# Performance work log

Hardware: AMD Instinct MI355X
Metric: run time of the kernel (lower is better)

The kernel has to match this reference:

```python
import jax, jax.numpy as jnp
import numpy as np
import math

B, T = 32, 64
VOCAB = 50005
EMB = 512
HID = 1024
SES = 1024
KNOW = 8785
NEG = math.exp(-100)

def _glorot(key, shape):
    fan_in, fan_out = shape[1], shape[0]
    lim = (6.0 / (fan_in + fan_out)) ** 0.5
    return jax.random.uniform(key, shape, jnp.float32, -lim, lim)

def setup_inputs() -> dict:
    key = jax.random.key(0)
    ks = jax.random.split(key, 16)
    inp = {}
    inp['ses_encoding'] = jax.random.normal(ks[0], (B, 1, SES), jnp.float32)
    inp['know_encoding'] = jax.random.normal(ks[1], (B, 1, SES), jnp.float32)
    inp['target'] = jax.random.randint(ks[2], (B, T), 0, 50000)
    inp['embed_w'] = jax.random.normal(ks[3], (VOCAB, EMB), jnp.float32) * 0.02
    # GRU params (PyTorch layout: W_ih [3H, E], W_hh [3H, H], gate order r,z,n)
    s = 1.0 / (HID ** 0.5)
    inp['W_ih'] = jax.random.uniform(ks[4], (3 * HID, EMB), jnp.float32, -s, s)
    inp['W_hh'] = jax.random.uniform(ks[5], (3 * HID, HID), jnp.float32, -s, s)
    inp['b_ih'] = jax.random.uniform(ks[6], (3 * HID,), jnp.float32, -s, s)
    inp['b_hh'] = jax.random.uniform(ks[7], (3 * HID,), jnp.float32, -s, s)
    inp['ses_to_dec_w'] = _glorot(ks[8], (HID, SES))
    inp['ses_to_dec_b'] = jnp.zeros((HID,), jnp.float32)
    inp['dec_inf_w'] = _glorot(ks[9], (2 * EMB, HID))
    inp['ses_inf_w'] = _glorot(ks[10], (2 * EMB, SES))
    inp['emb_inf_w'] = _glorot(ks[11], (2 * EMB, EMB))
    inp['emb_inf_b'] = jnp.zeros((2 * EMB,), jnp.float32)
    inp['W1'] = jax.random.normal(ks[12], (VOCAB, SES), jnp.float32) * 0.02
    inp['W2'] = jax.random.normal(ks[13], (VOCAB, SES), jnp.float32) * 0.02
    inp['W3'] = jax.random.normal(ks[14], (VOCAB, 2 * EMB), jnp.float32) * 0.02
    inp['W4'] = jax.random.normal(ks[15], (VOCAB, EMB), jnp.float32) * 0.02
    inp['know_vote_w'] = _glorot(jax.random.fold_in(key, 99), (KNOW, SES))
    return inp

def _gru_step(x, h, W_ih, W_hh, b_ih, b_hh):
    # x: [B,E], h: [B,H]
    gi = x @ W_ih.T + b_ih
    gh = h @ W_hh.T + b_hh
    ir, iz, inn = jnp.split(gi, 3, axis=-1)
    hr, hz, hn = jnp.split(gh, 3, axis=-1)
    r = jax.nn.sigmoid(ir + hr)
    z = jax.nn.sigmoid(iz + hz)
    n = jnp.tanh(inn + r * hn)
    return (1.0 - z) * h + z * n  # torch: h' = (1-z)*n + z*h with torch z; note torch formula

def _gru_step_torch(x, h, W_ih, W_hh, b_ih, b_hh):
    gi = x @ W_ih.T + b_ih
    gh = h @ W_hh.T + b_hh
    ir, iz, inn = jnp.split(gi, 3, axis=-1)
    hr, hz, hn = jnp.split(gh, 3, axis=-1)
    r = jax.nn.sigmoid(ir + hr)
    z = jax.nn.sigmoid(iz + hz)
    n = jnp.tanh(inn + r * hn)
    return (1.0 - z) * n + z * h

def reference(ses_encoding, know_encoding, target, embed_w, W_ih, W_hh, b_ih, b_hh,
              ses_to_dec_w, ses_to_dec_b, dec_inf_w, ses_inf_w, emb_inf_w, emb_inf_b,
              W1, W2, W3, W4, know_vote_w):
    ses = ses_encoding[:, 0, :]    # [B, SES]
    know = know_encoding[:, 0, :]  # [B, SES]
    target_emb = embed_w[target]   # [B, T, E]

    h0 = jnp.tanh(ses @ ses_to_dec_w.T + ses_to_dec_b)  # [B, H]

    # time-invariant pieces
    ses_inf_vec = ses @ ses_inf_w.T                      # [B, 2E]
    l1 = ses @ W1.T                                      # [B, V]
    l2 = know @ W2.T                                     # [B, V]
    # knowledge mixture log-probs (constant over time)
    ks = know @ know_vote_w.T                            # [B, KNOW]
    ks = ks[:, :-1]                                      # drop last -> [B, KNOW-1]
    pad_l = jnp.full((ks.shape[0], 10), NEG, ks.dtype)
    pad_r = jnp.full((ks.shape[0], VOCAB - 10 - (KNOW - 1)), NEG, ks.dtype)
    know_scores = jnp.concatenate([pad_l, ks, pad_r], axis=1)  # [B, V]
    know_probs = jax.nn.log_softmax(know_scores, axis=-1)      # [B, V]
    gate_const = l1 + l2                                 # [B, V]

    def step(h, emb_t):
        # emb_t: [B, E]
        h_new = _gru_step_torch(emb_t, h, W_ih, W_hh, b_ih, b_hh)  # [B, H]
        dec_hid_vec = h_new @ dec_inf_w.T                          # [B, 2E]
        target_inf = emb_t @ emb_inf_w.T + emb_inf_b               # [B, 2E]
        total = dec_hid_vec + ses_inf_vec + target_inf             # [B, 2E]
        mx = jnp.max(total.reshape(total.shape[0], EMB, 2), axis=-1)  # maxout -> [B, E]
        logits = mx @ embed_w.T                                    # shared embedding -> [B, V]
        hid_probs = jax.nn.log_softmax(logits, axis=-1)
        l3 = h_new @ W3.T                                          # note: W3 applied to hid_o [B,H]... but W3 is [V,2E]
        l4 = emb_t @ W4.T                                          # [B, V]
        gate = jax.nn.sigmoid(gate_const + l3 + l4)                # [B, V]
        final = gate * hid_probs + (1.0 - gate) * know_probs       # [B, V]
        return h_new, final

    # target_emb time-major for scan
    _, outs = jax.lax.scan(step, h0, jnp.swapaxes(target_emb, 0, 1))
    final_scores_all = jnp.swapaxes(outs, 0, 1)  # [B, T, V]
    return final_scores_all
```

## Files before the change

### kernel.cpp

```cpp
#include <hip/hip_runtime.h>

constexpr int VOC  = 50005;
constexpr int VOCP = 50048;
constexpr int VOCP2= 50176;
constexpr int NTM  = 391;
constexpr int NTMP = 400;
constexpr int KSN  = 8784;
constexpr float NPAD = 41221.0f;

typedef unsigned short u16;
typedef __attribute__((ext_vector_type(4))) float f32x4;
typedef __attribute__((ext_vector_type(8))) short bf16x8;

__device__ __forceinline__ float dot4(float4 a, float4 b) {
    return a.x*b.x + a.y*b.y + a.z*b.z + a.w*b.w;
}
__device__ __forceinline__ float sigmoidf_(float x) { return 1.0f / (1.0f + expf(-x)); }
__device__ __forceinline__ u16 f2bf(float f) {
    unsigned x = __float_as_uint(f);
    return (u16)((x + 0x7FFFu + ((x >> 16) & 1u)) >> 16);
}
__device__ __forceinline__ float bf2f(u16 u) { return __uint_as_float(((unsigned)u) << 16); }
__device__ __forceinline__ bf16x8 pack8(float4 lo, float4 hi) {
    union { bf16x8 v; unsigned u[4]; } r;
    r.u[0] = f2bf(lo.x) | ((unsigned)f2bf(lo.y) << 16);
    r.u[1] = f2bf(lo.z) | ((unsigned)f2bf(lo.w) << 16);
    r.u[2] = f2bf(hi.x) | ((unsigned)f2bf(hi.y) << 16);
    r.u[3] = f2bf(hi.z) | ((unsigned)f2bf(hi.w) << 16);
    return r.v;
}
template<int AUX>
__device__ __forceinline__ void gload_lds16x(const void* g, void* l) {
    __builtin_amdgcn_global_load_lds((const __attribute__((address_space(1))) unsigned int*)g,
                                     (__attribute__((address_space(3))) unsigned int*)l, 16, 0, AUX);
}
__device__ __forceinline__ void gload_lds16(const void* g, void* l) { gload_lds16x<0>(g, l); }
__device__ __forceinline__ void store_u16_sc(u16* p, u16 v) {
    asm volatile("global_store_short %0, %1, off sc0 sc1" :: "v"(p), "v"((unsigned)v) : "memory");
}
__device__ __forceinline__ void cvt4(const float* src, u16* dst) {
    float4 v = *(const float4*)src;
    unsigned lo = f2bf(v.x) | ((unsigned)f2bf(v.y) << 16);
    unsigned hi = f2bf(v.z) | ((unsigned)f2bf(v.w) << 16);
    *(uint2*)dst = make_uint2(lo, hi);
}

__global__ __launch_bounds__(256) void k_cvt(const float* __restrict__ src, u16* __restrict__ dst,
                                             int ncols, int sld, int dld) {
    int row = blockIdx.x;
    int c = (blockIdx.y * 256 + threadIdx.x) * 4;
    if (c >= ncols) return;
    cvt4(src + (size_t)row * sld + c, dst + (size_t)row * dld + c);
}

__global__ __launch_bounds__(256) void k_bsk(const float* __restrict__ ses,
                                             const float* __restrict__ know,
                                             u16* __restrict__ Bsk) {
    int row = blockIdx.x;
    for (int c0 = threadIdx.x * 4; c0 < 2048; c0 += 1024) {
        uint2 val = make_uint2(0, 0);
        if (row < 32) {
            const float* srcp = (c0 < 1024) ? ses + (size_t)row * 1024 + c0
                                            : know + (size_t)row * 1024 + (c0 - 1024);
            float4 v = *(const float4*)srcp;
            val = make_uint2(f2bf(v.x) | ((unsigned)f2bf(v.y) << 16),
                             f2bf(v.z) | ((unsigned)f2bf(v.w) << 16));
        }
        *(uint2*)(Bsk + (size_t)row * 2048 + c0) = val;
    }
}

__global__ __launch_bounds__(128) void k_gather(const float* __restrict__ embed,
                                                const int* __restrict__ target,
                                                u16* __restrict__ BG) {
    int n = blockIdx.x;
    int row = target[n];
    int c = threadIdx.x * 4;
    cvt4(embed + (size_t)row * 512 + c, BG + (size_t)n * 1536 + 1024 + c);
}

__global__ __launch_bounds__(256) void k_h0_sesinf(const float* __restrict__ ses,
                                                   const float* __restrict__ sdw,
                                                   const float* __restrict__ sdb,
                                                   const float* __restrict__ siw,
                                                   float* __restrict__ h0,
                                                   float* __restrict__ sesinf) {
    int g = blockIdx.x * 256 + threadIdx.x;
    int b = g & 31;
    int jg = g >> 5;
    int j0 = jg * 4;
    const float4* s4 = (const float4*)(ses + (size_t)b * 1024);
    const float4* wa[4];
    const float4* wc[4];
#pragma unroll
    for (int r = 0; r < 4; ++r) {
        wa[r] = (const float4*)(sdw + (size_t)(j0 + r) * 1024);
        wc[r] = (const float4*)(siw + (size_t)(j0 + r) * 1024);
    }
    float a[4] = {0, 0, 0, 0}, c[4] = {0, 0, 0, 0};
    for (int kq = 0; kq < 256; ++kq) {
        float4 sv = s4[kq];
#pragma unroll
        for (int r = 0; r < 4; ++r) { a[r] += dot4(sv, wa[r][kq]); c[r] += dot4(sv, wc[r][kq]); }
    }
#pragma unroll
    for (int r = 0; r < 4; ++r) {
        h0[b * 1024 + j0 + r] = tanhf(a[r] + sdb[j0 + r]);
        sesinf[b * 1024 + j0 + r] = c[r];
    }
}

__global__ __launch_bounds__(256) void k_lseknow(const float* __restrict__ ks,
                                                 float* __restrict__ lsek) {
    int b = blockIdx.x;
    int t = threadIdx.x;
    __shared__ float sm[256];
    float m = -1e30f;
    for (int j = t; j < KSN; j += 256) m = fmaxf(m, ks[(size_t)b * KSN + j]);
    sm[t] = m;
    __syncthreads();
    for (int s = 128; s > 0; s >>= 1) { if (t < s) sm[t] = fmaxf(sm[t], sm[t + s]); __syncthreads(); }
    m = fmaxf(sm[0], 0.0f);
    __syncthreads();
    float s = 0.0f;
    for (int j = t; j < KSN; j += 256) s += expf(ks[(size_t)b * KSN + j] - m);
    sm[t] = s;
    __syncthreads();
    for (int r = 128; r > 0; r >>= 1) { if (t < r) sm[t] += sm[t + r]; __syncthreads(); }
    if (t == 0) lsek[b] = m + logf(sm[0] + NPAD * expf(0.0f - m));
}

template<int MODE>
__global__ __launch_bounds__(128) void k_sk32(const float* __restrict__ A1,
                                              const float* __restrict__ A2,
                                              const u16* __restrict__ Bsk,
                                              float* __restrict__ outp) {
    const int lane = threadIdx.x & 63;
    const int w = threadIdx.x >> 6;
    const int lrow = lane & 15;
    const int kg = lane >> 4;
    constexpr int K = (MODE == 0) ? 2048 : 1024;
    constexpr int bc0 = (MODE == 0) ? 0 : 1024;
    const int rowmax = (MODE == 0) ? (VOC - 1) : (KSN - 1);
    const int vb = blockIdx.x * 64 + w * 32;
    const int r0 = min(vb + lrow, rowmax);
    const int r1 = min(vb + 16 + lrow, rowmax);
    f32x4 acc[2][2] = {{{0.f,0.f,0.f,0.f},{0.f,0.f,0.f,0.f}},
                       {{0.f,0.f,0.f,0.f},{0.f,0.f,0.f,0.f}}};
    for (int k0 = 0; k0 < K; k0 += 32) {
        int kc = k0 + kg * 8;
        const float* s0;
        const float* s1;
        if (MODE == 0 && k0 >= 1024) {
            s0 = A2 + (size_t)r0 * 1024 + (kc - 1024);
            s1 = A2 + (size_t)r1 * 1024 + (kc - 1024);
        } else {
            s0 = A1 + (size_t)r0 * 1024 + kc;
            s1 = A1 + (size_t)r1 * 1024 + kc;
        }
        bf16x8 af0 = pack8(*(const float4*)s0, *(const float4*)(s0 + 4));
        bf16x8 af1 = pack8(*(const float4*)s1, *(const float4*)(s1 + 4));
        bf16x8 b0 = *(const bf16x8*)(Bsk + (size_t)lrow * 2048 + bc0 + kc);
        bf16x8 b1 = *(const bf16x8*)(Bsk + (size_t)(16 + lrow) * 2048 + bc0 + kc);
        acc[0][0] = __builtin_amdgcn_mfma_f32_16x16x32_bf16(af0, b0, acc[0][0], 0, 0, 0);
        acc[0][1] = __builtin_amdgcn_mfma_f32_16x16x32_bf16(af0, b1, acc[0][1], 0, 0, 0);
        acc[1][0] = __builtin_amdgcn_mfma_f32_16x16x32_bf16(af1, b0, acc[1][0], 0, 0, 0);
        acc[1][1] = __builtin_amdgcn_mfma_f32_16x16x32_bf16(af1, b1, acc[1][1], 0, 0, 0);
    }
    const int rg = kg * 4;
#pragma unroll
    for (int mi = 0; mi < 2; ++mi)
#pragma unroll
        for (int ni = 0; ni < 2; ++ni)
#pragma unroll
            for (int r = 0; r < 4; ++r) {
                int v = vb + mi * 16 + rg + r;
                int b = ni * 16 + lrow;
                if (MODE == 0) outp[(size_t)b * VOCP2 + v] = acc[mi][ni][r];
                else if (v < KSN) outp[(size_t)b * KSN + v] = acc[mi][ni][r];
            }
}

template<int EPI>
__global__ __launch_bounds__(256) void gemm_bt(
    const u16* __restrict__ A, int lda,
    const u16* __restrict__ B, int ldb, int K,
    const float* __restrict__ p0, const float* __restrict__ p1,
    float* __restrict__ q0, u16* __restrict__ q1, float* __restrict__ q3)
{
    __shared__ u16 Asm[128 * 64];
    __shared__ u16 Bsm[128 * 64];
    const int tid = threadIdx.x;
    const int lane = tid & 63;
    const int w = tid >> 6;
    const int wm = w >> 1, wn = w & 1;
    const int nt = blockIdx.x, mt = blockIdx.y;

    f32x4 acc[4][4];
#pragma unroll
    for (int i = 0; i < 4; ++i)
#pragma unroll
        for (int j = 0; j < 4; ++j) acc[i][j] = (f32x4){0.f, 0.f, 0.f, 0.f};

    for (int kt = 0; kt < K; kt += 64) {
#pragma unroll
        for (int p = 0; p < 4; ++p) {
            int flat = (w * 4 + p) * 64 + lane;
            int row = flat >> 3, slot = flat & 7;
            int ss = slot ^ (row & 7);
            gload_lds16(A + (size_t)(mt * 128 + row) * lda + kt + ss * 8, Asm + flat * 8);
            gload_lds16(B + (size_t)(nt * 128 + row) * ldb + kt + ss * 8, Bsm + flat * 8);
        }
        __syncthreads();
#pragma unroll
        for (int kc = 0; kc < 2; ++kc) {
            bf16x8 af[4], bfr[4];
#pragma unroll
            for (int mi = 0; mi < 4; ++mi) {
                int row = wm * 64 + mi * 16 + (lane & 15);
                int bcol = kc * 64 + ((lane >> 4) << 4);
                af[mi] = *(const bf16x8*)((const char*)Asm + row * 128 + (bcol ^ ((row & 7) << 4)));
            }
#pragma unroll
            for (int ni = 0; ni < 4; ++ni) {
                int row = wn * 64 + ni * 16 + (lane & 15);
                int bcol = kc * 64 + ((lane >> 4) << 4);
                bfr[ni] = *(const bf16x8*)((const char*)Bsm + row * 128 + (bcol ^ ((row & 7) << 4)));
            }
#pragma unroll
            for (int mi = 0; mi < 4; ++mi)
#pragma unroll
                for (int ni = 0; ni < 4; ++ni)
                    acc[mi][ni] = __builtin_amdgcn_mfma_f32_16x16x32_bf16(af[mi], bfr[ni], acc[mi][ni], 0, 0, 0);
        }
        __syncthreads();
    }

    const int cl = lane & 15;
    const int rg = (lane >> 4) << 2;

    if constexpr (EPI == 0) {
#pragma unroll
        for (int mi = 0; mi < 4; ++mi) {
            int m0 = mt * 128 + wm * 64 + mi * 16 + rg;
            float4 bias = *(const float4*)(p0 + m0);
#pragma unroll
            for (int ni = 0; ni < 4; ++ni) {
                int n = nt * 128 + wn * 64 + ni * 16 + cl;
                float4 v;
                v.x = acc[mi][ni][0] + bias.x; v.y = acc[mi][ni][1] + bias.y;
                v.z = acc[mi][ni][2] + bias.z; v.w = acc[mi][ni][3] + bias.w;
                *(float4*)(q0 + (size_t)n * 3072 + m0) = v;
            }
        }
    }
    if constexpr (EPI == 1) {
#pragma unroll
        for (int mi = 0; mi < 4; ++mi) {
            int m0 = mt * 128 + wm * 64 + mi * 16 + rg;
            float4 eb4 = *(const float4*)(p1 + m0);
#pragma unroll
            for (int ni = 0; ni < 4; ++ni) {
                int n = nt * 128 + wn * 64 + ni * 16 + cl;
                int b = n >> 6;
                float v0 = acc[mi][ni][0] + p0[b * 1024 + m0 + 0] + eb4.x;
                float v1 = acc[mi][ni][1] + p0[b * 1024 + m0 + 1] + eb4.y;
                float v2 = acc[mi][ni][2] + p0[b * 1024 + m0 + 2] + eb4.z;
                float v3 = acc[mi][ni][3] + p0[b * 1024 + m0 + 3] + eb4.w;
                unsigned pk = f2bf(fmaxf(v0, v1)) | ((unsigned)f2bf(fmaxf(v2, v3)) << 16);
                *(unsigned*)(q1 + (size_t)n * 512 + (m0 >> 1)) = pk;
            }
        }
    }
    if constexpr (EPI == 3) {
        __shared__ float redm[2][128];
        __shared__ float reds[2][128];
#pragma unroll
        for (int mi = 0; mi < 4; ++mi) {
            int v0 = mt * 128 + wm * 64 + mi * 16 + rg;
#pragma unroll
            for (int ni = 0; ni < 4; ++ni) {
                int n = nt * 128 + wn * 64 + ni * 16 + cl;
                unsigned lo = f2bf(acc[mi][ni][0]) | ((unsigned)f2bf(acc[mi][ni][1]) << 16);
                unsigned hi = f2bf(acc[mi][ni][2]) | ((unsigned)f2bf(acc[mi][ni][3]) << 16);
                *(uint2*)(q1 + (size_t)n * VOCP + v0) = make_uint2(lo, hi);
            }
        }
#pragma unroll
        for (int ni = 0; ni < 4; ++ni) {
            float lm = -1e30f;
#pragma unroll
            for (int mi = 0; mi < 4; ++mi) {
                int v0 = mt * 128 + wm * 64 + mi * 16 + rg;
#pragma unroll
                for (int r = 0; r < 4; ++r)
                    if (v0 + r < VOC) lm = fmaxf(lm, acc[mi][ni][r]);
            }
            lm = fmaxf(lm, __shfl_xor(lm, 16));
            lm = fmaxf(lm, __shfl_xor(lm, 32));
            float s = 0.0f;
#pragma unroll
            for (int mi = 0; mi < 4; ++mi) {
                int v0 = mt * 128 + wm * 64 + mi * 16 + rg;
#pragma unroll
                for (int r = 0; r < 4; ++r)
                    if (v0 + r < VOC) s += expf(acc[mi][ni][r] - lm);
            }
            s += __shfl_xor(s, 16);
            s += __shfl_xor(s, 32);
            if (lane < 16) {
                redm[wm][wn * 64 + ni * 16 + lane] = lm;
                reds[wm][wn * 64 + ni * 16 + lane] = s;
            }
        }
        __syncthreads();
        if (tid < 128) {
            float m0_ = redm[0][tid], m1_ = redm[1][tid];
            float m = fmaxf(m0_, m1_);
            float s = reds[0][tid] * expf(m0_ - m) + reds[1][tid] * expf(m1_ - m);
            int n = nt * 128 + tid;
            q0[(size_t)n * NTMP + mt] = m;
            q3[(size_t)n * NTMP + mt] = s;
        }
    }
}

__global__ __launch_bounds__(512, 1) void gemm_gate8(
    const u16* __restrict__ A,
    const u16* __restrict__ B,
    const float* __restrict__ gc2,
    unsigned char* __restrict__ g8)
{
    __shared__ __align__(16) char smem[131072];
    const int tid = threadIdx.x;
    const int lane = tid & 63;
    const int w = tid >> 6;
    const int wm = w >> 2;
    const int wn = w & 3;
    const int lrow = lane & 15;
    const int g = lane >> 4;

    int bid = blockIdx.x;
    int wg = (bid & 7) * 196 + (bid >> 3);
    int mt = wg >> 3;
    int nt = wg & 7;
    const size_t arow0 = (size_t)mt * 256;
    const size_t brow0 = (size_t)nt * 256;

    auto stageA = [&](int T, int h) {
        char* dst = smem + (T & 1) * 65536 + h * 16384;
        const u16* src = A + (arow0 + h * 128) * 1536 + T * 64;
#pragma unroll
        for (int q = 0; q < 2; ++q) {
            int flat = q * 512 + tid;
            int r = flat >> 3, s = flat & 7;
            int ss = s ^ (r & 7);
            gload_lds16(src + (size_t)r * 1536 + ss * 8, dst + flat * 16);
        }
    };
    auto stageB = [&](int T, int h) {
        char* dst = smem + (T & 1) * 65536 + 32768 + h * 16384;
        const u16* src = B + (brow0 + h * 128) * 1536 + T * 64;
#pragma unroll
        for (int q = 0; q < 2; ++q) {
            int flat = q * 512 + tid;
            int r = flat >> 3, s = flat & 7;
            int ss = s ^ (r & 7);
            gload_lds16(src + (size_t)r * 1536 + ss * 8, dst + flat * 16);
        }
    };

    f32x4 acc[8][4];
#pragma unroll
    for (int i = 0; i < 8; ++i)
#pragma unroll
        for (int j = 0; j < 4; ++j) acc[i][j] = (f32x4){0.f, 0.f, 0.f, 0.f};

    bf16x8 bf[4][2];
    auto loadB_ = [&](int d) {
        char* Bb = smem + d * 65536 + 32768 + (wn >> 1) * 16384;
#pragma unroll
        for (int ni = 0; ni < 4; ++ni) {
            int r = (wn & 1) * 64 + ni * 16 + lrow;
#pragma unroll
            for (int kk = 0; kk < 2; ++kk)
                bf[ni][kk] = *(const bf16x8*)(Bb + r * 128 + ((kk * 64 + g * 16) ^ ((r & 7) << 4)));
        }
    };

#define GPH2(D, Q, LB, STG)                                                           \
    {                                                                                 \
        STG;                                                                          \
        if (LB) loadB_(D);                                                            \
        bf16x8 af[2][2];                                                              \
        char* Ab = smem + (D) * 65536 + wm * 16384;                                   \
        _Pragma("unroll") for (int mi = 0; mi < 2; ++mi) {                            \
            int r = ((Q) * 2 + mi) * 16 + lrow;                                       \
            _Pragma("unroll") for (int kk = 0; kk < 2; ++kk)                          \
                af[mi][kk] = *(const bf16x8*)(Ab + r * 128 +                          \
                                ((kk * 64 + g * 16) ^ ((r & 7) << 4)));               \
        }                                                                             \
        asm volatile("s_waitcnt lgkmcnt(0)" ::: "memory");                            \
        __builtin_amdgcn_sched_barrier(0);                                            \
        __builtin_amdgcn_s_setprio(1);                                                \
        _Pragma("unroll") for (int kk = 0; kk < 2; ++kk)                              \
            _Pragma("unroll") for (int mi = 0; mi < 2; ++mi)                          \
                _Pragma("unroll") for (int ni = 0; ni < 4; ++ni)                      \
                    acc[(Q) * 2 + mi][ni] = __builtin_amdgcn_mfma_f32_16x16x32_bf16(  \
                        af[mi][kk], bf[ni][kk], acc[(Q) * 2 + mi][ni], 0, 0, 0);      \
        __builtin_amdgcn_s_setprio(0);                                                \
    }
#define BARR  __builtin_amdgcn_sched_barrier(0); __builtin_amdgcn_s_barrier(); \
              __builtin_amdgcn_sched_barrier(0)
#define VM4 asm volatile("s_waitcnt vmcnt(4)" ::: "memory"); __builtin_amdgcn_sched_barrier(0)
#define VM0 asm volatile("s_waitcnt vmcnt(0)" ::: "memory"); __builtin_amdgcn_sched_barrier(0)
#define NOPX (void)0

    stageB(0, 0); stageB(0, 1); stageA(0, 0); stageA(0, 1); stageB(1, 0); stageB(1, 1);
    VM4;
    BARR;

    for (int i = 0; i < 11; ++i) {
        int T0 = 2 * i, T1 = 2 * i + 1;
        GPH2(0, 0, true,  stageA(T1, 0));
        GPH2(0, 1, false, stageA(T1, 1));
        BARR;
        GPH2(0, 2, false, stageB(T0 + 2, 0));
        GPH2(0, 3, false, stageB(T0 + 2, 1));
        VM4; BARR;
        GPH2(1, 0, true,  stageA(T0 + 2, 0));
        GPH2(1, 1, false, stageA(T0 + 2, 1));
        BARR;
        GPH2(1, 2, false, stageB(T1 + 2, 0));
        GPH2(1, 3, false, stageB(T1 + 2, 1));
        VM4; BARR;
    }
    GPH2(0, 0, true,  stageA(23, 0));
    GPH2(0, 1, false, stageA(23, 1));
    BARR;
    GPH2(0, 2, false, NOPX);
    GPH2(0, 3, false, NOPX);
    VM0; BARR;
    GPH2(1, 0, true,  NOPX);
    GPH2(1, 1, false, NOPX);
    GPH2(1, 2, false, NOPX);
    GPH2(1, 3, false, NOPX);
#undef GPH2
#undef BARR
#undef VM4
#undef VM0
#undef NOPX

    const int rg = g << 2;
    const int b = nt * 4 + wn;
    const float* gcrow = gc2 + (size_t)b * VOCP2;
#pragma unroll
    for (int m = 0; m < 8; ++m) {
        int v0 = mt * 256 + wm * 128 + m * 16 + rg;
        float4 gcv = *(const float4*)(gcrow + v0);
#pragma unroll
        for (int ni = 0; ni < 4; ++ni) {
            int n = nt * 256 + wn * 64 + ni * 16 + lrow;
            unsigned pk = 0;
#pragma unroll
            for (int r = 0; r < 4; ++r) {
                float garg = acc[m][ni][r] + ((const float*)&gcv)[r];
                float gate = 1.0f / (1.0f + expf(-garg));
                pk |= ((unsigned)(int)(gate * 255.0f + 0.5f)) << (8 * r);
            }
            *(unsigned*)(g8 + (size_t)n * VOCP2 + v0) = pk;
        }
    }
}

__global__ __launch_bounds__(256, 1) void k_gru_f(const u16* __restrict__ WhhB,
                                                  const float* __restrict__ GI,
                                                  const float* __restrict__ bhh,
                                                  const u16* __restrict__ h0b,
                                                  u16* __restrict__ BG,
                                                  unsigned* __restrict__ flags,
                                                  const float* __restrict__ embed,
                                                  const float* __restrict__ W3,
                                                  const float* __restrict__ W4,
                                                  const float* __restrict__ dw,
                                                  const float* __restrict__ ew,
                                                  u16* __restrict__ Aemb,
                                                  u16* __restrict__ A34,
                                                  u16* __restrict__ Adwew) {
    __shared__ __align__(16) char smem[163840];
    const int tid = threadIdx.x;

    if (blockIdx.x >= 64) {
        const long gtid = (long)(blockIdx.x - 64) * 256 + tid;
        const long gstr = 192L * 256;
        for (long i = gtid; i < (long)VOC * 128; i += gstr) {
            int row = (int)(i >> 7), c4 = ((int)i & 127) * 4;
            cvt4(embed + (size_t)row * 512 + c4, Aemb + (size_t)row * 512 + c4);
        }
        for (long i = gtid; i < (long)VOC * 256; i += gstr) {
            int row = (int)(i >> 8), c4 = ((int)i & 255) * 4;
            cvt4(W3 + (size_t)row * 1024 + c4, A34 + (size_t)row * 1536 + c4);
        }
        for (long i = gtid; i < (long)VOC * 128; i += gstr) {
            int row = (int)(i >> 7), c4 = ((int)i & 127) * 4;
            cvt4(W4 + (size_t)row * 512 + c4, A34 + (size_t)row * 1536 + 1024 + c4);
        }
        for (long i = gtid; i < 1024L * 256; i += gstr) {
            int row = (int)(i >> 8), c4 = ((int)i & 255) * 4;
            cvt4(dw + (size_t)row * 1024 + c4, Adwew + (size_t)row * 1536 + c4);
        }
        for (long i = gtid; i < 1024L * 128; i += gstr) {
            int row = (int)(i >> 7), c4 = ((int)i & 127) * 4;
            cvt4(ew + (size_t)row * 512 + c4, Adwew + (size_t)row * 1536 + 1024 + c4);
        }
        for (long i = gtid; i < (long)(VOCP2 - VOC) * 768; i += gstr) {
            int row = VOC + (int)(i / 768), c = (int)(i % 768);
            ((unsigned*)(A34 + (size_t)row * 1536))[c] = 0;
        }
        for (long i = gtid; i < (long)(VOCP - VOC) * 256; i += gstr) {
            int row = VOC + (int)(i >> 8), c = (int)i & 255;
            ((unsigned*)(Aemb + (size_t)row * 512))[c] = 0;
        }
        return;
    }

    const int lane = tid & 63;
    const int w = tid >> 6;
    const int jb = blockIdx.x;
    const int j0 = jb * 16;
    const int jl = tid & 15, bp = tid >> 4;
    const int je = j0 + jl;
    const float bh0 = bhh[je], bh1 = bhh[1024 + je], bh2 = bhh[2048 + je];
    char* Bbase = smem + 98304 + w * 16384;

#pragma unroll
    for (int it = 0; it < 24; ++it) {
        int flat = (it * 4 + w) * 64 + lane;
        int r = flat >> 7, s = flat & 127;
        int ss = s ^ (r & 7);
        int gr = (r >> 4) * 1024 + j0 + (r & 15);
        gload_lds16(WhhB + (size_t)gr * 1024 + ss * 8, smem + (size_t)flat * 16);
    }

    float hpv[2];
#pragma unroll
    for (int rb = 0; rb < 2; ++rb)
        hpv[rb] = bf2f(h0b[(size_t)(bp * 2 + rb) * 1024 + je]);

    const int lrow = lane & 15;
    const int ksel = lane >> 4;

    for (int t = 0; t < 64; ++t) {
        const u16* hsrc = (t == 0) ? h0b : BG + (size_t)(t - 1) * 1536;
        const size_t hstr = (t == 0) ? 1024 : (size_t)64 * 1536;

#pragma unroll
        for (int c = 0; c < 4; ++c) {
            char* dst = Bbase + c * 4096;
            int kq0 = w * 256 + c * 64;
#pragma unroll
            for (int q = 0; q < 4; ++q) {
                int flat = q * 64 + lane;
                int r = flat >> 3, s = flat & 7;
                int ss = s ^ (r & 7);
                gload_lds16x<0x11>(hsrc + (size_t)r * hstr + kq0 + ss * 8,
                                   dst + (size_t)flat * 16);
            }
        }
        float gi0[2], gi1[2], gi2[2];
#pragma unroll
        for (int rb = 0; rb < 2; ++rb) {
            const float* gp = GI + ((size_t)((bp * 2 + rb) * 64 + t)) * 3072 + je;
            gi0[rb] = gp[0]; gi1[rb] = gp[1024]; gi2[rb] = gp[2048];
        }
        if (t == 0) {
            __syncthreads();
        } else {
            asm volatile("s_waitcnt vmcnt(0)" ::: "memory");
        }
        __builtin_amdgcn_sched_barrier(0);

        f32x4 acc[3][2];
#pragma unroll
        for (int mi = 0; mi < 3; ++mi)
#pragma unroll
            for (int ni = 0; ni < 2; ++ni) acc[mi][ni] = (f32x4){0.f, 0.f, 0.f, 0.f};

#pragma unroll
        for (int c = 0; c < 4; ++c) {
            char* Bb = Bbase + c * 4096;
#pragma unroll
            for (int ks = 0; ks < 2; ++ks) {
                int kb = ks * 64 + ksel * 16;
                bf16x8 bfr[2];
#pragma unroll
                for (int ni = 0; ni < 2; ++ni) {
                    int br = ni * 16 + lrow;
                    bfr[ni] = *(const bf16x8*)(Bb + br * 128 + (kb ^ ((br & 7) << 4)));
                }
                int kA = w * 512 + c * 128 + kb;
#pragma unroll
                for (int mi = 0; mi < 3; ++mi) {
                    int ar = mi * 16 + lrow;
                    bf16x8 af = *(const bf16x8*)(smem + ar * 2048 + (kA ^ ((ar & 7) << 4)));
#pragma unroll
                    for (int ni = 0; ni < 2; ++ni)
                        acc[mi][ni] = __builtin_amdgcn_mfma_f32_16x16x32_bf16(af, bfr[ni], acc[mi][ni], 0, 0, 0);
                }
            }
        }

        float (*epiw)[33] = (float(*)[33])Bbase;
        asm volatile("s_waitcnt lgkmcnt(0)" ::: "memory");
        __builtin_amdgcn_sched_barrier(0);
        {
            const int rg = (lane >> 4) << 2;
#pragma unroll
            for (int mi = 0; mi < 3; ++mi)
#pragma unroll
                for (int ni = 0; ni < 2; ++ni) {
                    int m0 = mi * 16 + rg;
                    int cb = ni * 16 + lrow;
#pragma unroll
                    for (int r = 0; r < 4; ++r) epiw[m0 + r][cb] = acc[mi][ni][r];
                }
        }
        asm volatile("s_waitcnt lgkmcnt(0)" ::: "memory");
        __builtin_amdgcn_s_barrier();

#pragma unroll
        for (int rb = 0; rb < 2; ++rb) {
            int b = bp * 2 + rb;
            float s0 = 0.f, s1 = 0.f, s2 = 0.f;
#pragma unroll
            for (int ww = 0; ww < 4; ++ww) {
                float (*ep)[33] = (float(*)[33])(smem + 98304 + ww * 16384);
                s0 += ep[jl][b]; s1 += ep[16 + jl][b]; s2 += ep[32 + jl][b];
            }
            float rr = sigmoidf_(gi0[rb] + s0 + bh0);
            float zz = sigmoidf_(gi1[rb] + s1 + bh1);
            float nn = tanhf(gi2[rb] + rr * (s2 + bh2));
            float hnew = (1.0f - zz) * nn + zz * hpv[rb];
            hpv[rb] = hnew;
            store_u16_sc(BG + ((size_t)(b * 64 + t)) * 1536 + je, f2bf(hnew));
        }

        if (t < 63) {
            asm volatile("s_waitcnt vmcnt(0)" ::: "memory");
            __syncthreads();
            if (tid == 0)
                __hip_atomic_store(&flags[jb], (unsigned)(t + 1),
                                   __ATOMIC_RELAXED, __HIP_MEMORY_SCOPE_AGENT);
            unsigned tgt = (unsigned)(t + 1);
            while (true) {
                unsigned v = __hip_atomic_load(&flags[lane],
                                               __ATOMIC_RELAXED, __HIP_MEMORY_SCOPE_AGENT);
                if (__all(v >= tgt)) break;
                __builtin_amdgcn_s_sleep(1);
            }
            __builtin_amdgcn_sched_barrier(0);
        }
    }
}

__global__ __launch_bounds__(256) void k_lse(const float* __restrict__ pmax,
                                             const float* __restrict__ psum,
                                             float* __restrict__ lse) {
    int n = blockIdx.x;
    int t = threadIdx.x;
    __shared__ float sm[256];
    const float* pm = pmax + (size_t)n * NTMP;
    const float* ps = psum + (size_t)n * NTMP;
    float m = -1e30f;
    for (int p = t; p < NTM; p += 256) m = fmaxf(m, pm[p]);
    sm[t] = m;
    __syncthreads();
    for (int s = 128; s > 0; s >>= 1) { if (t < s) sm[t] = fmaxf(sm[t], sm[t + s]); __syncthreads(); }
    m = sm[0];
    __syncthreads();
    float s = 0.0f;
    for (int p = t; p < NTM; p += 256) s += ps[p] * expf(pm[p] - m);
    sm[t] = s;
    __syncthreads();
    for (int r = 128; r > 0; r >>= 1) { if (t < r) sm[t] += sm[t + r]; __syncthreads(); }
    if (t == 0) lse[n] = m + logf(sm[0]);
}

__global__ __launch_bounds__(256) void k_final(const u16* __restrict__ Lb,
                                               const unsigned char* __restrict__ g8,
                                               const float* __restrict__ lse,
                                               const float* __restrict__ ks,
                                               const float* __restrict__ lsek,
                                               float* __restrict__ out) {
    int n = blockIdx.y;
    int b = n >> 6;
    float lsen = lse[n], lkb = lsek[b];
    int base = blockIdx.x * 2048;
#pragma unroll
    for (int i = 0; i < 8; ++i) {
        int v = base + i * 256 + threadIdx.x;
        if (v < VOC) {
            float L = bf2f(Lb[(size_t)n * VOCP + v]);
            float g = g8[(size_t)n * VOCP2 + v] * (1.0f / 255.0f);
            float kp = ((v >= 10 && v < 10 + KSN) ? ks[(size_t)b * KSN + (v - 10)] : 0.0f) - lkb;
            out[(size_t)n * VOC + v] = g * (L - lsen) + (1.0f - g) * kp;
        }
    }
}

extern "C" void kernel_launch(void* const* d_in, const int* in_sizes, int n_in,
                              void* d_out, int out_size, void* d_ws, size_t ws_size,
                              hipStream_t stream) {
    const float* ses    = (const float*)d_in[0];
    const float* know   = (const float*)d_in[1];
    const int*   target = (const int*)d_in[2];
    const float* embed  = (const float*)d_in[3];
    const float* Wih    = (const float*)d_in[4];
    const float* Whh    = (const float*)d_in[5];
    const float* bih    = (const float*)d_in[6];
    const float* bhh    = (const float*)d_in[7];
    const float* sdw    = (const float*)d_in[8];
    const float* sdb    = (const float*)d_in[9];
    const float* dw     = (const float*)d_in[10];
    const float* siw    = (const float*)d_in[11];
    const float* ew     = (const float*)d_in[12];
    const float* eb     = (const float*)d_in[13];
    const float* W1     = (const float*)d_in[14];
    const float* W2     = (const float*)d_in[15];
    const float* W3     = (const float*)d_in[16];
    const float* W4     = (const float*)d_in[17];
    const float* kvw    = (const float*)d_in[18];

    char* ws = (char*)d_ws;
    size_t o = 0;
    auto alloc = [&](size_t bytes) { char* r = ws + o; o += (bytes + 255) & ~(size_t)255; return r; };
    u16*   Aemb  = (u16*)  alloc((size_t)VOCP * 512 * 2);
    u16*   A34   = (u16*)  alloc((size_t)VOCP2 * 1536 * 2);
    u16*   Adwew = (u16*)  alloc((size_t)1024 * 1536 * 2);
    u16*   Wihb  = (u16*)  alloc((size_t)3072 * 512 * 2);
    u16*   WhhB  = (u16*)  alloc((size_t)3072 * 1024 * 2);
    u16*   h0b   = (u16*)  alloc((size_t)32 * 1024 * 2);
    u16*   BG    = (u16*)  alloc((size_t)2048 * 1536 * 2);
    u16*   BL    = (u16*)  alloc((size_t)2048 * 512 * 2);
    float* GI    = (float*)alloc((size_t)2048 * 3072 * 4);
    float* h0    = (float*)alloc((size_t)32 * 1024 * 4);
    float* sesinf= (float*)alloc((size_t)32 * 1024 * 4);
    float* gc    = (float*)alloc((size_t)32 * VOCP2 * 4);
    float* ksb   = (float*)alloc((size_t)32 * KSN * 4);
    float* lsek  = (float*)alloc(256);
    float* lse   = (float*)alloc((size_t)2048 * 4);
    unsigned* flags = (unsigned*)alloc(256);
    float* pmax  = (float*)alloc((size_t)2048 * NTMP * 4);
    float* psum  = (float*)alloc((size_t)2048 * NTMP * 4);
    unsigned char* g8 = (unsigned char*)alloc((size_t)2048 * VOCP2);
    u16*   Lb    = (u16*)  alloc((size_t)2048 * VOCP * 2);
    u16*   Bsk   = (u16*)  alloc((size_t)128 * 2048 * 2);
    float* out = (float*)d_out;

    hipMemsetAsync(flags, 0, 256, stream);

    k_cvt<<<dim3(3072, 1), 256, 0, stream>>>(Wih, Wihb, 512, 512, 512);
    k_cvt<<<dim3(3072, 1), 256, 0, stream>>>(Whh, WhhB, 1024, 1024, 1024);
    k_bsk<<<dim3(128), 256, 0, stream>>>(ses, know, Bsk);
    k_gather<<<dim3(2048), 128, 0, stream>>>(embed, target, BG);
    k_h0_sesinf<<<dim3(32), 256, 0, stream>>>(ses, sdw, sdb, siw, h0, sesinf);
    k_cvt<<<dim3(32, 1), 256, 0, stream>>>(h0, h0b, 1024, 1024, 1024);

    k_sk32<0><<<dim3(VOCP2 / 64), 128, 0, stream>>>(W1, W2, Bsk, gc);
    k_sk32<1><<<dim3((KSN + 63) / 64), 128, 0, stream>>>(kvw, nullptr, Bsk, ksb);
    k_lseknow<<<dim3(32), 256, 0, stream>>>(ksb, lsek);

    gemm_bt<0><<<dim3(16, 24), 256, 0, stream>>>(Wihb, 512, BG + 1024, 1536, 512,
                                                 bih, nullptr, GI, nullptr, nullptr);
    k_gru_f<<<dim3(256), 256, 0, stream>>>(WhhB, GI, bhh, h0b, BG, flags,
                                           embed, W3, W4, dw, ew, Aemb, A34, Adwew);
    gemm_bt<1><<<dim3(16, 8), 256, 0, stream>>>(Adwew, 1536, BG, 1536, 1536,
                                                sesinf, eb, nullptr, BL, nullptr);
    gemm_gate8<<<dim3(1568), 512, 0, stream>>>(A34, BG, gc, g8);
    gemm_bt<3><<<dim3(16, NTM), 256, 0, stream>>>(Aemb, 512, BL, 512, 512,
                                                  nullptr, nullptr, pmax, Lb, psum);
    k_lse<<<dim3(2048), 256, 0, stream>>>(pmax, psum, lse);
    k_final<<<dim3(25, 2048), 256, 0, stream>>>(Lb, g8, lse, ksb, lsek, out);
}
```

Measured before the change: 1.529 ms.

## Fold session/knowledge score GEMMs into idle GRU helper blocks

The two standalone k_sk32 launches (the W1/W2 gate-constant scores and the knowledge-vote scores) are removed. Their work now runs in the 192 helper blocks of the persistent GRU kernel, alongside the weight conversions, so it overlaps the latency-bound serial GRU recurrence. Tasks are widened to 128 rows over 4 waves, and the conversion loops now handle 16 floats per thread instead of 4. The risk is that the helper blocks take longer and compete with the GRU blocks for memory bandwidth, which could lengthen the critical path.

```diff
diff --git a/kernel.cpp b/kernel.cpp
--- a/kernel.cpp
+++ b/kernel.cpp
@@ -43,6 +43,67 @@
     unsigned lo = f2bf(v.x) | ((unsigned)f2bf(v.y) << 16);
     unsigned hi = f2bf(v.z) | ((unsigned)f2bf(v.w) << 16);
     *(uint2*)dst = make_uint2(lo, hi);
+}
+__device__ __forceinline__ void cvt64(const float* src, u16* dst) {
+    float4 a = *(const float4*)src;
+    float4 b = *(const float4*)(src + 4);
+    float4 c = *(const float4*)(src + 8);
+    float4 d = *(const float4*)(src + 12);
+    uint2 pa = make_uint2(f2bf(a.x) | ((unsigned)f2bf(a.y) << 16), f2bf(a.z) | ((unsigned)f2bf(a.w) << 16));
+    uint2 pb = make_uint2(f2bf(b.x) | ((unsigned)f2bf(b.y) << 16), f2bf(b.z) | ((unsigned)f2bf(b.w) << 16));
+    uint2 pc = make_uint2(f2bf(c.x) | ((unsigned)f2bf(c.y) << 16), f2bf(c.z) | ((unsigned)f2bf(c.w) << 16));
+    uint2 pd = make_uint2(f2bf(d.x) | ((unsigned)f2bf(d.y) << 16), f2bf(d.z) | ((unsigned)f2bf(d.w) << 16));
+    *(uint2*)dst = pa; *(uint2*)(dst + 4) = pb; *(uint2*)(dst + 8) = pc; *(uint2*)(dst + 12) = pd;
+}
+
+template<int MODE>
+__device__ void sk32_task(int task, int tid,
+                          const float* __restrict__ A1, const float* __restrict__ A2,
+                          const u16* __restrict__ Bsk, float* __restrict__ outp) {
+    const int lane = tid & 63;
+    const int w4 = tid >> 6;
+    const int lrow = lane & 15;
+    const int kg = lane >> 4;
+    constexpr int K = (MODE == 0) ? 2048 : 1024;
+    constexpr int bc0 = (MODE == 0) ? 0 : 1024;
+    const int rowmax = (MODE == 0) ? (VOC - 1) : (KSN - 1);
+    const int vb = task * 128 + w4 * 32;
+    const int r0 = min(vb + lrow, rowmax);
+    const int r1 = min(vb + 16 + lrow, rowmax);
+    f32x4 acc[2][2] = {{{0.f,0.f,0.f,0.f},{0.f,0.f,0.f,0.f}},
+                       {{0.f,0.f,0.f,0.f},{0.f,0.f,0.f,0.f}}};
+    for (int k0 = 0; k0 < K; k0 += 32) {
+        int kc = k0 + kg * 8;
+        const float* s0;
+        const float* s1;
+        if (MODE == 0 && k0 >= 1024) {
+            s0 = A2 + (size_t)r0 * 1024 + (kc - 1024);
+            s1 = A2 + (size_t)r1 * 1024 + (kc - 1024);
+        } else {
+            s0 = A1 + (size_t)r0 * 1024 + kc;
+            s1 = A1 + (size_t)r1 * 1024 + kc;
+        }
+        bf16x8 af0 = pack8(*(const float4*)s0, *(const float4*)(s0 + 4));
+        bf16x8 af1 = pack8(*(const float4*)s1, *(const float4*)(s1 + 4));
+        bf16x8 b0 = *(const bf16x8*)(Bsk + (size_t)lrow * 2048 + bc0 + kc);
+        bf16x8 b1 = *(const bf16x8*)(Bsk + (size_t)(16 + lrow) * 2048 + bc0 + kc);
+        acc[0][0] = __builtin_amdgcn_mfma_f32_16x16x32_bf16(af0, b0, acc[0][0], 0, 0, 0);
+        acc[0][1] = __builtin_amdgcn_mfma_f32_16x16x32_bf16(af0, b1, acc[0][1], 0, 0, 0);
+        acc[1][0] = __builtin_amdgcn_mfma_f32_16x16x32_bf16(af1, b0, acc[1][0], 0, 0, 0);
+        acc[1][1] = __builtin_amdgcn_mfma_f32_16x16x32_bf16(af1, b1, acc[1][1], 0, 0, 0);
+    }
+    const int rg = kg * 4;
+#pragma unroll
+    for (int mi = 0; mi < 2; ++mi)
+#pragma unroll
+        for (int ni = 0; ni < 2; ++ni)
+#pragma unroll
+            for (int r = 0; r < 4; ++r) {
+                int v = vb + mi * 16 + rg + r;
+                int b = ni * 16 + lrow;
+                if (MODE == 0) outp[(size_t)b * VOCP2 + v] = acc[mi][ni][r];
+                else if (v < KSN) outp[(size_t)b * KSN + v] = acc[mi][ni][r];
+            }
 }
 
 __global__ __launch_bounds__(256) void k_cvt(const float* __restrict__ src, u16* __restrict__ dst,
@@ -128,57 +189,6 @@
     __syncthreads();
     for (int r = 128; r > 0; r >>= 1) { if (t < r) sm[t] += sm[t + r]; __syncthreads(); }
     if (t == 0) lsek[b] = m + logf(sm[0] + NPAD * expf(0.0f - m));
-}
-
-template<int MODE>
-__global__ __launch_bounds__(128) void k_sk32(const float* __restrict__ A1,
-                                              const float* __restrict__ A2,
-                                              const u16* __restrict__ Bsk,
-                                              float* __restrict__ outp) {
-    const int lane = threadIdx.x & 63;
-    const int w = threadIdx.x >> 6;
-    const int lrow = lane & 15;
-    const int kg = lane >> 4;
-    constexpr int K = (MODE == 0) ? 2048 : 1024;
-    constexpr int bc0 = (MODE == 0) ? 0 : 1024;
-    const int rowmax = (MODE == 0) ? (VOC - 1) : (KSN - 1);
-    const int vb = blockIdx.x * 64 + w * 32;
-    const int r0 = min(vb + lrow, rowmax);
-    const int r1 = min(vb + 16 + lrow, rowmax);
-    f32x4 acc[2][2] = {{{0.f,0.f,0.f,0.f},{0.f,0.f,0.f,0.f}},
-                       {{0.f,0.f,0.f,0.f},{0.f,0.f,0.f,0.f}}};
-    for (int k0 = 0; k0 < K; k0 += 32) {
-        int kc = k0 + kg * 8;
-        const float* s0;
-        const float* s1;
-        if (MODE == 0 && k0 >= 1024) {
-            s0 = A2 + (size_t)r0 * 1024 + (kc - 1024);
-            s1 = A2 + (size_t)r1 * 1024 + (kc - 1024);
-        } else {
-            s0 = A1 + (size_t)r0 * 1024 + kc;
-            s1 = A1 + (size_t)r1 * 1024 + kc;
-        }
-        bf16x8 af0 = pack8(*(const float4*)s0, *(const float4*)(s0 + 4));
-        bf16x8 af1 = pack8(*(const float4*)s1, *(const float4*)(s1 + 4));
-        bf16x8 b0 = *(const bf16x8*)(Bsk + (size_t)lrow * 2048 + bc0 + kc);
-        bf16x8 b1 = *(const bf16x8*)(Bsk + (size_t)(16 + lrow) * 2048 + bc0 + kc);
-        acc[0][0] = __builtin_amdgcn_mfma_f32_16x16x32_bf16(af0, b0, acc[0][0], 0, 0, 0);
-        acc[0][1] = __builtin_amdgcn_mfma_f32_16x16x32_bf16(af0, b1, acc[0][1], 0, 0, 0);
-        acc[1][0] = __builtin_amdgcn_mfma_f32_16x16x32_bf16(af1, b0, acc[1][0], 0, 0, 0);
-        acc[1][1] = __builtin_amdgcn_mfma_f32_16x16x32_bf16(af1, b1, acc[1][1], 0, 0, 0);
-    }
-    const int rg = kg * 4;
-#pragma unroll
-    for (int mi = 0; mi < 2; ++mi)
-#pragma unroll
-        for (int ni = 0; ni < 2; ++ni)
-#pragma unroll
-            for (int r = 0; r < 4; ++r) {
-                int v = vb + mi * 16 + rg + r;
-                int b = ni * 16 + lrow;
-                if (MODE == 0) outp[(size_t)b * VOCP2 + v] = acc[mi][ni][r];
-                else if (v < KSN) outp[(size_t)b * KSN + v] = acc[mi][ni][r];
-            }
 }
 
 template<int EPI>
@@ -484,6 +494,12 @@
                                                   const float* __restrict__ W4,
                                                   const float* __restrict__ dw,
                                                   const float* __restrict__ ew,
+                                                  const float* __restrict__ W1,
+                                                  const float* __restrict__ W2,
+                                                  const float* __restrict__ kvw,
+                                                  const u16* __restrict__ Bsk,
+                                                  float* __restrict__ gc,
+                                                  float* __restrict__ ksb,
                                                   u16* __restrict__ Aemb,
                                                   u16* __restrict__ A34,
                                                   u16* __restrict__ Adwew) {
@@ -491,27 +507,30 @@
     const int tid = threadIdx.x;
 
     if (blockIdx.x >= 64) {
-        const long gtid = (long)(blockIdx.x - 64) * 256 + tid;
+        const int hb = blockIdx.x - 64;
+        for (int t = hb; t < 392; t += 192) sk32_task<0>(t, tid, W1, W2, Bsk, gc);
+        for (int t = hb; t < 69; t += 192) sk32_task<1>(t, tid, kvw, nullptr, Bsk, ksb);
+        const long gtid = (long)hb * 256 + tid;
         const long gstr = 192L * 256;
-        for (long i = gtid; i < (long)VOC * 128; i += gstr) {
-            int row = (int)(i >> 7), c4 = ((int)i & 127) * 4;
-            cvt4(embed + (size_t)row * 512 + c4, Aemb + (size_t)row * 512 + c4);
-        }
-        for (long i = gtid; i < (long)VOC * 256; i += gstr) {
-            int row = (int)(i >> 8), c4 = ((int)i & 255) * 4;
-            cvt4(W3 + (size_t)row * 1024 + c4, A34 + (size_t)row * 1536 + c4);
-        }
-        for (long i = gtid; i < (long)VOC * 128; i += gstr) {
-            int row = (int)(i >> 7), c4 = ((int)i & 127) * 4;
-            cvt4(W4 + (size_t)row * 512 + c4, A34 + (size_t)row * 1536 + 1024 + c4);
-        }
-        for (long i = gtid; i < 1024L * 256; i += gstr) {
-            int row = (int)(i >> 8), c4 = ((int)i & 255) * 4;
-            cvt4(dw + (size_t)row * 1024 + c4, Adwew + (size_t)row * 1536 + c4);
-        }
-        for (long i = gtid; i < 1024L * 128; i += gstr) {
-            int row = (int)(i >> 7), c4 = ((int)i & 127) * 4;
-            cvt4(ew + (size_t)row * 512 + c4, Adwew + (size_t)row * 1536 + 1024 + c4);
+        for (long i = gtid; i < (long)VOC * 32; i += gstr) {
+            int row = (int)(i >> 5), c = ((int)i & 31) * 16;
+            cvt64(embed + (size_t)row * 512 + c, Aemb + (size_t)row * 512 + c);
+        }
+        for (long i = gtid; i < (long)VOC * 64; i += gstr) {
+            int row = (int)(i >> 6), c = ((int)i & 63) * 16;
+            cvt64(W3 + (size_t)row * 1024 + c, A34 + (size_t)row * 1536 + c);
+        }
+        for (long i = gtid; i < (long)VOC * 32; i += gstr) {
+            int row = (int)(i >> 5), c = ((int)i & 31) * 16;
+            cvt64(W4 + (size_t)row * 512 + c, A34 + (size_t)row * 1536 + 1024 + c);
+        }
+        for (long i = gtid; i < 1024L * 64; i += gstr) {
+            int row = (int)(i >> 6), c = ((int)i & 63) * 16;
+            cvt64(dw + (size_t)row * 1024 + c, Adwew + (size_t)row * 1536 + c);
+        }
+        for (long i = gtid; i < 1024L * 32; i += gstr) {
+            int row = (int)(i >> 5), c = ((int)i & 31) * 16;
+            cvt64(ew + (size_t)row * 512 + c, Adwew + (size_t)row * 1536 + 1024 + c);
         }
         for (long i = gtid; i < (long)(VOCP2 - VOC) * 768; i += gstr) {
             int row = VOC + (int)(i / 768), c = (int)(i % 768);
@@ -766,14 +785,13 @@
     k_h0_sesinf<<<dim3(32), 256, 0, stream>>>(ses, sdw, sdb, siw, h0, sesinf);
     k_cvt<<<dim3(32, 1), 256, 0, stream>>>(h0, h0b, 1024, 1024, 1024);
 
-    k_sk32<0><<<dim3(VOCP2 / 64), 128, 0, stream>>>(W1, W2, Bsk, gc);
-    k_sk32<1><<<dim3((KSN + 63) / 64), 128, 0, stream>>>(kvw, nullptr, Bsk, ksb);
-    k_lseknow<<<dim3(32), 256, 0, stream>>>(ksb, lsek);
-
     gemm_bt<0><<<dim3(16, 24), 256, 0, stream>>>(Wihb, 512, BG + 1024, 1536, 512,
                                                  bih, nullptr, GI, nullptr, nullptr);
     k_gru_f<<<dim3(256), 256, 0, stream>>>(WhhB, GI, bhh, h0b, BG, flags,
-                                           embed, W3, W4, dw, ew, Aemb, A34, Adwew);
+                                           embed, W3, W4, dw, ew,
+                                           W1, W2, kvw, Bsk, gc, ksb,
+                                           Aemb, A34, Adwew);
+    k_lseknow<<<dim3(32), 256, 0, stream>>>(ksb, lsek);
     gemm_bt<1><<<dim3(16, 8), 256, 0, stream>>>(Adwew, 1536, BG, 1536, 1536,
                                                 sesinf, eb, nullptr, BL, nullptr);
     gemm_gate8<<<dim3(1568), 512, 0, stream>>>(A34, BG, gc, g8);
```

Measured after the change: 1.394 ms, median of 2. 8.8% less time.
